# Performance work log

Hardware: AMD Instinct MI355X
Metric: run time of the kernel (lower is better)

Reference implementation:

```python
import jax, jax.numpy as jnp
import numpy as np

H, W, D = 56, 56, 28            # input_resolution
WS = (7, 7, 7)                  # window size (Wh, Ww, Wd)
SS = (3, 3, 3)                  # shift size
DIM = 96
NH = 3
HD = DIM // NH
N = WS[0] * WS[1] * WS[2]       # 343 tokens per window
NW = (H // WS[0]) * (W // WS[1]) * (D // WS[2])  # 256 windows


def _rel_pos_index():
    Wd, Wh, Ww = WS
    coords = np.stack(np.meshgrid(np.arange(Wd), np.arange(Wh), np.arange(Ww), indexing='ij'))
    cf = coords.reshape(3, -1)
    rel = (cf[:, :, None] - cf[:, None, :]).transpose(1, 2, 0)
    rel[:, :, 0] += Wd - 1
    rel[:, :, 1] += Wh - 1
    rel[:, :, 2] += Ww - 1
    rel[:, :, 0] *= (2 * Wh - 1) * (2 * Ww - 1)
    rel[:, :, 1] *= (2 * Ww - 1)
    return rel.sum(-1)  # (N, N)


def _attn_mask():
    img = np.zeros((H, W, D), np.float32)
    def slices(w, s):
        return (slice(0, -w), slice(-w, -s), slice(-s, None))
    cnt = 0
    for hs in slices(WS[0], SS[0]):
        for ws in slices(WS[1], SS[1]):
            for ds in slices(WS[2], SS[2]):
                img[hs, ws, ds] = cnt
                cnt += 1
    mw = img.reshape(H // WS[0], WS[0], W // WS[1], WS[1], D // WS[2], WS[2])
    mw = mw.transpose(0, 2, 4, 1, 3, 5).reshape(-1, N)  # (NW, N)
    am = mw[:, None, :] - mw[:, :, None]
    return np.where(am != 0, np.float32(-100.0), np.float32(0.0))


REL_IDX = jnp.asarray(_rel_pos_index())
ATTN_MASK = jnp.asarray(_attn_mask())  # (NW, N, N)


def _ln(x, g, b, eps=1e-5):
    m = x.mean(-1, keepdims=True)
    v = jnp.mean((x - m) ** 2, -1, keepdims=True)
    return (x - m) * jax.lax.rsqrt(v + eps) * g + b


def _forward(x, n1g, n1b, qkv_w, qkv_b, rpb, proj_w, proj_b,
             n2g, n2b, fc1_w, fc1_b, fc2_w, fc2_b):
    B, L, C = x.shape
    shortcut = x
    h = _ln(x, n1g, n1b).reshape(B, H, W, D, C)
    # cyclic shift
    h = jnp.roll(h, (-SS[0], -SS[1], -SS[2]), axis=(1, 2, 3))
    # window partition -> (B*NW, N, C)
    h = h.reshape(B, H // WS[0], WS[0], W // WS[1], WS[1], D // WS[2], WS[2], C)
    h = h.transpose(0, 1, 3, 5, 2, 4, 6, 7).reshape(-1, N, C)
    # qkv
    qkv = (h @ qkv_w + qkv_b).reshape(-1, N, 3, NH, HD).transpose(2, 0, 3, 1, 4)
    q, k, v = qkv[0] * (HD ** -0.5), qkv[1], qkv[2]  # (B*NW, NH, N, HD)
    attn = jnp.einsum('bhnd,bhmd->bhnm', q, k)
    bias = rpb[REL_IDX.reshape(-1)].reshape(N, N, NH).transpose(2, 0, 1)
    attn = attn + bias[None]
    # shifted-window mask
    attn = attn.reshape(B, NW, NH, N, N) + ATTN_MASK[None, :, None]
    attn = jax.nn.softmax(attn.reshape(-1, NH, N, N), axis=-1)
    o = jnp.einsum('bhnm,bhmd->bhnd', attn, v).transpose(0, 2, 1, 3).reshape(-1, N, C)
    o = o @ proj_w + proj_b
    # window reverse
    o = o.reshape(B, H // WS[0], W // WS[1], D // WS[2], WS[0], WS[1], WS[2], C)
    o = o.transpose(0, 1, 4, 2, 5, 3, 6, 7).reshape(B, H, W, D, C)
    o = jnp.roll(o, SS, axis=(1, 2, 3)).reshape(B, L, C)
    x = shortcut + o
    h2 = _ln(x, n2g, n2b)
    h2 = jax.nn.gelu(h2 @ fc1_w + fc1_b, approximate=False) @ fc2_w + fc2_b
    return x + h2


def setup_inputs() -> dict:
    key = jax.random.key(0)
    ks = jax.random.split(key, 6)
    C, FF = DIM, 4 * DIM
    f32 = jnp.float32
    return {
        'x': jax.random.normal(ks[0], (1, H * W * D, C), f32),
        'n1g': jnp.ones((C,), f32), 'n1b': jnp.zeros((C,), f32),
        'qkv_w': jax.random.normal(ks[1], (C, 3 * C), f32) * 0.02,
        'qkv_b': jnp.zeros((3 * C,), f32),
        'rpb': jax.random.normal(ks[2], ((2 * WS[0] - 1) * (2 * WS[1] - 1) * (2 * WS[2] - 1), NH), f32) * 0.02,
        'proj_w': jax.random.normal(ks[3], (C, C), f32) * 0.02,
        'proj_b': jnp.zeros((C,), f32),
        'n2g': jnp.ones((C,), f32), 'n2b': jnp.zeros((C,), f32),
        'fc1_w': jax.random.normal(ks[4], (C, FF), f32) * 0.02,
        'fc1_b': jnp.zeros((FF,), f32),
        'fc2_w': jax.random.normal(ks[5], (FF, C), f32) * 0.02,
        'fc2_b': jnp.zeros((C,), f32),
    }


def reference(x, n1g, n1b, qkv_w, qkv_b, rpb, proj_w, proj_b,
              n2g, n2b, fc1_w, fc1_b, fc2_w, fc2_b):
    return _forward(x, n1g, n1b, qkv_w, qkv_b, rpb, proj_w, proj_b,
                    n2g, n2b, fc1_w, fc1_b, fc2_w, fc2_b)
```

## Files before the change

kernel.cpp:

```cpp
#include <hip/hip_runtime.h>
#include <hip/hip_bf16.h>


#define L_TOK 87808

typedef unsigned int uint;
typedef __attribute__((ext_vector_type(8))) short short8;
typedef __attribute__((ext_vector_type(4))) float f32x4;

__device__ __forceinline__ float bflo(uint u){ union{uint x; float f;} a; a.x = u << 16; return a.f; }
__device__ __forceinline__ float bfhi(uint u){ union{uint x; float f;} a; a.x = u & 0xffff0000u; return a.f; }
__device__ __forceinline__ float bfval(unsigned short w){ union{uint x; float f;} a; a.x = (uint)w << 16; return a.f; }
__device__ __forceinline__ unsigned short f2bfbits(float f){
  union{float f; uint u;} a; a.f = f;
  uint u = a.u;
  u += 0x7fffu + ((u >> 16) & 1u);
  return (unsigned short)(u >> 16);
}
__device__ __forceinline__ unsigned short bfb(float f){
  __hip_bfloat16 h = __float2bfloat16(f);
  return *reinterpret_cast<unsigned short*>(&h);
}
__device__ __forceinline__ uint pkbf(float a, float b){
  return ((uint)bfb(b) << 16) | (uint)bfb(a);
}
__device__ __forceinline__ uint pack2(float a, float b){
  return ((uint)f2bfbits(b) << 16) | (uint)f2bfbits(a);
}
__device__ __forceinline__ uint4 pack8(const float* p){
  uint4 u;
  u.x = pack2(p[0], p[1]); u.y = pack2(p[2], p[3]);
  u.z = pack2(p[4], p[5]); u.w = pack2(p[6], p[7]);
  return u;
}
__device__ __forceinline__ uint4 pack8g(const float* gp){
  float t[8];
  *(float4*)&t[0] = *(const float4*)gp;
  *(float4*)&t[4] = *(const float4*)(gp + 4);
  return pack8(t);
}
__device__ __forceinline__ float gelu_f(float v){
  const float ax = fabsf(v) * 0.70710678118654752f;
  const float t  = 1.0f / (1.0f + 0.3275911f * ax);
  const float poly = t*(0.254829592f + t*(-0.284496736f + t*(1.421413741f +
                     t*(-1.453152027f + t*1.061405429f))));
  float erfv = 1.0f - poly * __expf(-ax*ax);
  erfv = copysignf(erfv, v);
  return 0.5f * v * (1.0f + erfv);
}
__device__ __forceinline__ uint gt_of_row(uint row){
  const uint win = row / 343u, n = row % 343u;
  const uint wh = win >> 5, ww = (win >> 2) & 7u, wd = win & 3u;
  const uint ih = n / 49u, rr = n % 49u, iw = rr / 7u, id = rr % 7u;
  uint gh = wh*7u + ih + 3u; if (gh >= 56u) gh -= 56u;
  uint gw = ww*7u + iw + 3u; if (gw >= 56u) gw -= 56u;
  uint gd = wd*7u + id + 3u; if (gd >= 28u) gd -= 28u;
  return ((gh*56u + gw)*28u + gd) * 96u;
}

__global__ __launch_bounds__(256)
void k_tr(const float* __restrict__ src, unsigned short* __restrict__ dst,
          int K, int N)
{
  const int idx = blockIdx.x * 256 + threadIdx.x;
  if (idx < K * N) {
    const int n = idx / K, k = idx % K;
    dst[idx] = f2bfbits(src[(size_t)k * N + n]);
  }
}

__global__ __launch_bounds__(256)
void k_mb(const float* __restrict__ rpbg, unsigned short* __restrict__ MB)
{
  const int idx = blockIdx.x * 256 + threadIdx.x;
  const int cls = idx / (3*352*352);
  const int rem = idx - cls * (3*352*352);
  const int h = rem / (352*352);
  const int rem2 = rem - h * (352*352);
  const int q = rem2 / 352;
  const int k = rem2 - q * 352;
  unsigned short v = 0xFF80;
  if (q < 343 && k < 343) {
    const int q0 = q/49, q1 = (q%49)/7, q2 = q%7;
    const int k0 = k/49, k1 = (k%49)/7, k2 = k%7;
    const int bq = q0*169 + q1*13 + q2;
    const int bk = k0*169 + k1*13 + k2;
    float bias = rpbg[(size_t)(bq - bk + 1098)*3 + h];
    int cq = 0, ck = 0;
    if (cls & 4) { cq += ((q0 < 4) ? 1 : 2)*9; ck += ((k0 < 4) ? 1 : 2)*9; }
    if (cls & 2) { cq += ((q1 < 4) ? 1 : 2)*3; ck += ((k1 < 4) ? 1 : 2)*3; }
    if (cls & 1) { cq += (q2 < 4) ? 1 : 2;     ck += (k2 < 4) ? 1 : 2; }
    if (cq != ck) bias -= 100.0f;
    v = f2bfbits(bias);
  }
  MB[idx] = v;
}

__global__ __launch_bounds__(256)
void k_qkv_ln(const float* __restrict__ x,
              const float* __restrict__ n1g,
              const float* __restrict__ n1b,
              const unsigned short* __restrict__ qkvwt,
              const float* __restrict__ bias, size_t headStride,
              __hip_bfloat16* __restrict__ qb,
              __hip_bfloat16* __restrict__ kb,
              __hip_bfloat16* __restrict__ vb)
{
  __shared__ __align__(16) unsigned short As[64][104];
  __shared__ uint srcOff[64];
  __shared__ float gLds[96], bLds[96];
  __shared__ float pSum[256], pSq[256];
  __shared__ float mLds[64], sLds[64];

  const int tid = threadIdx.x;
  const int wave = tid >> 6, lane = tid & 63;
  const int row0 = blockIdx.x * 64;

  if (tid < 64) srcOff[tid] = gt_of_row((uint)(row0 + tid));
  if (tid < 96) { gLds[tid] = n1g[tid]; bLds[tid] = n1b[tid]; }
  __syncthreads();

  for (int i = tid; i < 768; i += 256) {
    const int r = i / 12, kk = (i % 12) * 8;
    *(uint4*)&As[r][kk] = pack8g(x + srcOff[r] + kk);
  }
  __syncthreads();

  {
    const int r = tid & 63, seg = tid >> 6;
    float s = 0.0f, sq = 0.0f;
    #pragma unroll
    for (int j3 = 0; j3 < 3; ++j3) {
      const uint4 u = *(const uint4*)&As[r][seg*24 + j3*8];
      float v[8];
      v[0]=bflo(u.x); v[1]=bfhi(u.x); v[2]=bflo(u.y); v[3]=bfhi(u.y);
      v[4]=bflo(u.z); v[5]=bfhi(u.z); v[6]=bflo(u.w); v[7]=bfhi(u.w);
      #pragma unroll
      for (int j = 0; j < 8; ++j) { s += v[j]; sq += v[j]*v[j]; }
    }
    pSum[tid] = s; pSq[tid] = sq;
  }
  __syncthreads();
  if (tid < 64) {
    const float s  = pSum[tid] + pSum[tid+64] + pSum[tid+128] + pSum[tid+192];
    const float sq = pSq[tid] + pSq[tid+64] + pSq[tid+128] + pSq[tid+192];
    const float mean = s * (1.0f/96.0f);
    mLds[tid] = mean;
    sLds[tid] = rsqrtf(sq*(1.0f/96.0f) - mean*mean + 1e-5f);
  }
  __syncthreads();
  for (int i = tid; i < 768; i += 256) {
    const int r = i / 12, kk = (i % 12) * 8;
    uint4 u = *(uint4*)&As[r][kk];
    const float m = mLds[r], sc = sLds[r];
    float v[8];
    v[0]=bflo(u.x); v[1]=bfhi(u.x); v[2]=bflo(u.y); v[3]=bfhi(u.y);
    v[4]=bflo(u.z); v[5]=bfhi(u.z); v[6]=bflo(u.w); v[7]=bfhi(u.w);
    #pragma unroll
    for (int j = 0; j < 8; ++j) v[j] = (v[j] - m)*sc*gLds[kk+j] + bLds[kk+j];
    *(uint4*)&As[r][kk] = pack8(v);
  }
  __syncthreads();

  f32x4 acc[18];
  #pragma unroll
  for (int i = 0; i < 18; ++i) acc[i] = (f32x4){0.f, 0.f, 0.f, 0.f};
  const int ml = lane & 15, q8 = (lane >> 4) * 8;
  #pragma unroll
  for (int kc = 0; kc < 3; ++kc) {
    const short8 a = *(const short8*)&As[wave*16 + ml][kc*32 + q8];
    #pragma unroll
    for (int nt = 0; nt < 18; ++nt) {
      const short8 b = *(const short8*)(qkvwt + (size_t)(nt*16 + ml)*96 + kc*32 + q8);
      acc[nt] = __builtin_amdgcn_mfma_f32_16x16x32_bf16(a, b, acc[nt], 0, 0, 0);
    }
  }

  const float qscale = 0.17677669529663687f;
  #pragma unroll
  for (int nt = 0; nt < 18; ++nt) {
    const int nbase = nt * 16;
    const int part = nbase / 96;
    const int rem  = nbase - part * 96;
    const int h    = rem >> 5;
    const int dbase= rem & 31;
    __hip_bfloat16* base = (part == 0) ? qb : ((part == 1) ? kb : vb);
    __hip_bfloat16* dst = base + (size_t)h * headStride;
    const float bv = bias[nbase + ml];
    #pragma unroll
    for (int r = 0; r < 4; ++r) {
      const size_t row = (size_t)(row0 + wave*16 + (lane >> 4)*4 + r);
      float v = acc[nt][r] + bv;
      if (part == 0) v *= qscale;
      dst[row*32 + dbase + ml] = __float2bfloat16(v);
    }
  }
}

template<bool BF16OUT>
__global__ __launch_bounds__(256, 4)
void k_attn_v10(const __hip_bfloat16* __restrict__ qg,
                const __hip_bfloat16* __restrict__ kg,
                const __hip_bfloat16* __restrict__ vg,
                size_t headStride,
                const unsigned short* __restrict__ MB,
                void* __restrict__ obp)
{
  __shared__ __align__(16) unsigned short vt[32*344 + 16];
  __shared__ __align__(16) unsigned short Pc[4][16*56];
  __shared__ float lred[4][16];

  const int tid = threadIdx.x;
  const int wave = tid >> 6, lane = tid & 63;
  const uint win = blockIdx.x;
  const int hh = (int)blockIdx.y;
  const int mtBase = (int)blockIdx.z * 11;
  const size_t wbase = (size_t)hh * headStride + (size_t)win * (343*32);
  const unsigned short* qw = (const unsigned short*)qg + wbase;
  const unsigned short* kw = (const unsigned short*)kg + wbase;
  const unsigned short* vw = (const unsigned short*)vg + wbase;

  const uint wh = win >> 5, ww = (win >> 2) & 7u, wd = win & 3u;
  const int cls = ((wh == 7u) ? 4 : 0) | ((ww == 7u) ? 2 : 0) | ((wd == 3u) ? 1 : 0);
  const unsigned short* MBh = MB + ((size_t)cls*3 + hh) * (352*352);

  for (int t = tid; t < 343; t += 256) {
    const uint4* src = (const uint4*)(vw + (size_t)t*32);
    #pragma unroll
    for (int c4 = 0; c4 < 4; ++c4) {
      const uint4 u = src[c4];
      const int d = c4*8;
      vt[(d+0)*344 + t] = (unsigned short)(u.x & 0xffffu);
      vt[(d+1)*344 + t] = (unsigned short)(u.x >> 16);
      vt[(d+2)*344 + t] = (unsigned short)(u.y & 0xffffu);
      vt[(d+3)*344 + t] = (unsigned short)(u.y >> 16);
      vt[(d+4)*344 + t] = (unsigned short)(u.z & 0xffffu);
      vt[(d+5)*344 + t] = (unsigned short)(u.z >> 16);
      vt[(d+6)*344 + t] = (unsigned short)(u.w & 0xffffu);
      vt[(d+7)*344 + t] = (unsigned short)(u.w >> 16);
    }
  }
  if (tid < 32) vt[tid*344 + 343] = 0;
  if (tid < 16) vt[32*344 + tid] = 0;
  __syncthreads();

  const int ml = lane & 15, g = lane >> 4, g8 = g*8;
  unsigned short* Pw = &Pc[wave][0];

  for (int mt = mtBase + wave; mt < mtBase + 11; mt += 4) {
    const int q = mt*16 + ml;
    const short8 qf = *(const short8*)(qw + (size_t)q*32 + g8);
    const unsigned short* MBq = MBh + (size_t)q * 352;
    float l = 0.0f;
    f32x4 o0 = {0.f,0.f,0.f,0.f}, o1 = {0.f,0.f,0.f,0.f};

    for (int kc = 0; kc < 11; ++kc) {
      const short8 kf0 = *(const short8*)(kw + (size_t)(kc*32 + ml)*32 + g8);
      const short8 kf1 = *(const short8*)(kw + (size_t)(kc*32 + 16 + ml)*32 + g8);
      f32x4 s0 = __builtin_amdgcn_mfma_f32_16x16x32_bf16(kf0, qf, (f32x4){0.f,0.f,0.f,0.f}, 0, 0, 0);
      f32x4 s1 = __builtin_amdgcn_mfma_f32_16x16x32_bf16(kf1, qf, (f32x4){0.f,0.f,0.f,0.f}, 0, 0, 0);

      const ushort4 u0 = *(const ushort4*)(MBq + kc*32 + 4*g);
      const ushort4 u1 = *(const ushort4*)(MBq + kc*32 + 16 + 4*g);

      float p0 = __expf(s0[0] + bfval(u0.x));
      float p1 = __expf(s0[1] + bfval(u0.y));
      float p2 = __expf(s0[2] + bfval(u0.z));
      float p3 = __expf(s0[3] + bfval(u0.w));
      float p4 = __expf(s1[0] + bfval(u1.x));
      float p5 = __expf(s1[1] + bfval(u1.y));
      float p6 = __expf(s1[2] + bfval(u1.z));
      float p7 = __expf(s1[3] + bfval(u1.w));
      l += ((p0 + p1) + (p2 + p3)) + ((p4 + p5) + (p6 + p7));

      uint2 wlo, whi;
      wlo.x = pkbf(p0, p1); wlo.y = pkbf(p2, p3);
      whi.x = pkbf(p4, p5); whi.y = pkbf(p6, p7);
      *(uint2*)&Pw[ml*56 + 4*g]      = wlo;
      *(uint2*)&Pw[ml*56 + 16 + 4*g] = whi;

      const short8 pf  = *(const short8*)&Pw[ml*56 + g8];
      const short8 vf0 = *(const short8*)&vt[(size_t)ml*344 + kc*32 + g8];
      const short8 vf1 = *(const short8*)&vt[(size_t)(16 + ml)*344 + kc*32 + g8];
      o0 = __builtin_amdgcn_mfma_f32_16x16x32_bf16(pf, vf0, o0, 0, 0, 0);
      o1 = __builtin_amdgcn_mfma_f32_16x16x32_bf16(pf, vf1, o1, 0, 0, 0);
    }

    l += __shfl_xor(l, 16);
    l += __shfl_xor(l, 32);
    if (g == 0) lred[wave][ml] = 1.0f / l;
    const float4 li = *(const float4*)&lred[wave][4*g];
    #pragma unroll
    for (int r = 0; r < 4; ++r) {
      const int row = mt*16 + 4*g + r;
      if (row < 343) {
        const size_t base = ((size_t)win*343 + (uint)row)*96 + hh*32;
        if (BF16OUT) {
          __hip_bfloat16* op = (__hip_bfloat16*)obp + base;
          op[ml]      = __float2bfloat16(o0[r] * li[r]);
          op[16 + ml] = __float2bfloat16(o1[r] * li[r]);
        } else {
          float* op = (float*)obp + base;
          op[ml]      = o0[r] * li[r];
          op[16 + ml] = o1[r] * li[r];
        }
      }
    }
  }
}

__global__ __launch_bounds__(256, 2)
void k_pm(const __hip_bfloat16* __restrict__ obb,
          const unsigned short* __restrict__ pwt,
          const float* __restrict__ pb,
          const float* __restrict__ xin,
          const float* __restrict__ n2g,
          const float* __restrict__ n2b,
          const unsigned short* __restrict__ w1t,
          const float* __restrict__ b1,
          const unsigned short* __restrict__ w2t,
          const float* __restrict__ b2,
          float* __restrict__ out)
{
  __shared__ __align__(16) unsigned short As[64][104];
  __shared__ __align__(16) unsigned short Rs[64][104];
  __shared__ __align__(16) unsigned short inter[64][200];
  __shared__ uint gtO[64];
  float* scr  = (float*)&inter[0][0];
  float* pSum = scr;
  float* pSq  = scr + 256;
  float* gL   = scr + 512;
  float* bL   = scr + 608;
  float* mL   = scr + 704;
  float* sL   = scr + 768;

  const int tid = threadIdx.x;
  const int wave = tid >> 6, lane = tid & 63;
  const int row0 = blockIdx.x * 64;
  const int ml = lane & 15, g = lane >> 4, g8 = g*8;

  if (tid < 64) gtO[tid] = gt_of_row((uint)(row0 + tid));
  if (tid < 96) { gL[tid] = n2g[tid]; bL[tid] = n2b[tid]; }
  for (int i = tid; i < 768; i += 256) {
    const int r = i / 12, kk = (i % 12) * 8;
    *(uint4*)&As[r][kk] = *(const uint4*)(obb + (size_t)(row0 + r)*96 + kk);
  }
  __syncthreads();

  {
    short8 paf[3];
    #pragma unroll
    for (int kc = 0; kc < 3; ++kc)
      paf[kc] = *(const short8*)&As[wave*16 + ml][kc*32 + g8];
    f32x4 acc[6];
    #pragma unroll
    for (int i = 0; i < 6; ++i) acc[i] = (f32x4){0.f, 0.f, 0.f, 0.f};
    #pragma unroll
    for (int kc = 0; kc < 3; ++kc)
      #pragma unroll
      for (int nt = 0; nt < 6; ++nt) {
        const short8 b = *(const short8*)(pwt + (size_t)(nt*16 + ml)*96 + kc*32 + g8);
        acc[nt] = __builtin_amdgcn_mfma_f32_16x16x32_bf16(paf[kc], b, acc[nt], 0, 0, 0);
      }
    #pragma unroll
    for (int nt = 0; nt < 6; ++nt) {
      const int col = nt*16 + ml;
      const float pbv = pb[col];
      #pragma unroll
      for (int r = 0; r < 4; ++r) {
        const int rl = wave*16 + 4*g + r;
        const float v = acc[nt][r] + pbv + xin[(size_t)gtO[rl] + col];
        Rs[rl][col] = f2bfbits(v);
      }
    }
  }
  __syncthreads();

  {
    const int r = tid & 63, seg = tid >> 6;
    float s = 0.0f, sq = 0.0f;
    #pragma unroll
    for (int j3 = 0; j3 < 3; ++j3) {
      const uint4 u = *(const uint4*)&Rs[r][seg*24 + j3*8];
      float v[8];
      v[0]=bflo(u.x); v[1]=bfhi(u.x); v[2]=bflo(u.y); v[3]=bfhi(u.y);
      v[4]=bflo(u.z); v[5]=bfhi(u.z); v[6]=bflo(u.w); v[7]=bfhi(u.w);
      #pragma unroll
      for (int j = 0; j < 8; ++j) { s += v[j]; sq += v[j]*v[j]; }
    }
    pSum[tid] = s; pSq[tid] = sq;
  }
  __syncthreads();
  if (tid < 64) {
    const float s  = pSum[tid] + pSum[tid+64] + pSum[tid+128] + pSum[tid+192];
    const float sq = pSq[tid] + pSq[tid+64] + pSq[tid+128] + pSq[tid+192];
    const float mean = s * (1.0f/96.0f);
    mL[tid] = mean;
    sL[tid] = rsqrtf(sq*(1.0f/96.0f) - mean*mean + 1e-5f);
  }
  __syncthreads();
  for (int i = tid; i < 768; i += 256) {
    const int r = i / 12, kk = (i % 12) * 8;
    uint4 u = *(uint4*)&Rs[r][kk];
    const float m = mL[r], sc = sL[r];
    float v[8];
    v[0]=bflo(u.x); v[1]=bfhi(u.x); v[2]=bflo(u.y); v[3]=bfhi(u.y);
    v[4]=bflo(u.z); v[5]=bfhi(u.z); v[6]=bflo(u.w); v[7]=bfhi(u.w);
    #pragma unroll
    for (int j = 0; j < 8; ++j) v[j] = (v[j] - m)*sc*gL[kk+j] + bL[kk+j];
    *(uint4*)&As[r][kk] = pack8(v);
  }
  __syncthreads();

  short8 af[4][3];
  #pragma unroll
  for (int mt = 0; mt < 4; ++mt)
    #pragma unroll
    for (int kc = 0; kc < 3; ++kc)
      af[mt][kc] = *(const short8*)&As[mt*16 + ml][kc*32 + g8];

  const int rb = 32 * (wave >> 1);
  const int cb = 48 * (wave & 1);
  f32x4 acc2[2][3];
  #pragma unroll
  for (int i = 0; i < 2; ++i)
    #pragma unroll
    for (int nt = 0; nt < 3; ++nt)
      acc2[i][nt] = (f32x4){0.f, 0.f, 0.f, 0.f};

  #pragma unroll
  for (int H = 0; H < 2; ++H) {
    if (H) __syncthreads();

    const int nbg = H*192 + 48*wave;
    const int cl0 = 48*wave;
    short8 bf[3][3];
    #pragma unroll
    for (int nt = 0; nt < 3; ++nt)
      #pragma unroll
      for (int kc = 0; kc < 3; ++kc)
        bf[nt][kc] = *(const short8*)(w1t + (size_t)(nbg + 16*nt + ml)*96 + kc*32 + g8);

    f32x4 acc[4][3];
    #pragma unroll
    for (int mt = 0; mt < 4; ++mt)
      #pragma unroll
      for (int nt = 0; nt < 3; ++nt)
        acc[mt][nt] = (f32x4){0.f, 0.f, 0.f, 0.f};

    #pragma unroll
    for (int kc = 0; kc < 3; ++kc)
      #pragma unroll
      for (int nt = 0; nt < 3; ++nt)
        #pragma unroll
        for (int mt = 0; mt < 4; ++mt)
          acc[mt][nt] = __builtin_amdgcn_mfma_f32_16x16x32_bf16(af[mt][kc], bf[nt][kc], acc[mt][nt], 0, 0, 0);

    #pragma unroll
    for (int nt = 0; nt < 3; ++nt) {
      const float b1v = b1[nbg + 16*nt + ml];
      const int c = cl0 + 16*nt + ml;
      #pragma unroll
      for (int mt = 0; mt < 4; ++mt) {
        #pragma unroll
        for (int r = 0; r < 4; ++r) {
          inter[mt*16 + 4*g + r][c] = f2bfbits(gelu_f(acc[mt][nt][r] + b1v));
        }
      }
    }
    __syncthreads();

    #pragma unroll
    for (int kcl = 0; kcl < 6; ++kcl) {
      const short8 a0 = *(const short8*)&inter[rb + ml][kcl*32 + g8];
      const short8 a1 = *(const short8*)&inter[rb + 16 + ml][kcl*32 + g8];
      #pragma unroll
      for (int nt = 0; nt < 3; ++nt) {
        const short8 b = *(const short8*)(w2t + (size_t)(cb + 16*nt + ml)*384 + H*192 + kcl*32 + g8);
        acc2[0][nt] = __builtin_amdgcn_mfma_f32_16x16x32_bf16(a0, b, acc2[0][nt], 0, 0, 0);
        acc2[1][nt] = __builtin_amdgcn_mfma_f32_16x16x32_bf16(a1, b, acc2[1][nt], 0, 0, 0);
      }
    }
  }

  #pragma unroll
  for (int i = 0; i < 2; ++i) {
    #pragma unroll
    for (int nt = 0; nt < 3; ++nt) {
      const int col = cb + 16*nt + ml;
      const float b2v = b2[col];
      #pragma unroll
      for (int r = 0; r < 4; ++r) {
        const int rl = rb + 16*i + 4*g + r;
        out[(size_t)gtO[rl] + col] = acc2[i][nt][r] + b2v + bfval(Rs[rl][col]);
      }
    }
  }
}

__global__ __launch_bounds__(256)
void k_proj(const float* __restrict__ A,
            const unsigned short* __restrict__ pwt,
            const float* __restrict__ bias,
            const float* __restrict__ xin,
            __hip_bfloat16* __restrict__ xres)
{
  __shared__ __align__(16) unsigned short As[128][104];
  const int tid = threadIdx.x;
  const int wave = tid >> 6, lane = tid & 63;
  const int row0 = blockIdx.x * 128;

  for (int i = tid; i < 1536; i += 256) {
    const int r = i / 12, kk = (i % 12) * 8;
    *(uint4*)&As[r][kk] = pack8g(A + (size_t)(row0 + r)*96 + kk);
  }
  __syncthreads();

  f32x4 acc[2][6];
  #pragma unroll
  for (int mt = 0; mt < 2; ++mt)
    #pragma unroll
    for (int i = 0; i < 6; ++i) acc[mt][i] = (f32x4){0.f, 0.f, 0.f, 0.f};
  const int ml = lane & 15, q8 = (lane >> 4) * 8;
  #pragma unroll
  for (int kc = 0; kc < 3; ++kc) {
    const short8 a0 = *(const short8*)&As[wave*32 + ml][kc*32 + q8];
    const short8 a1 = *(const short8*)&As[wave*32 + 16 + ml][kc*32 + q8];
    #pragma unroll
    for (int nt = 0; nt < 6; ++nt) {
      const short8 b = *(const short8*)(pwt + (size_t)(nt*16 + ml)*96 + kc*32 + q8);
      acc[0][nt] = __builtin_amdgcn_mfma_f32_16x16x32_bf16(a0, b, acc[0][nt], 0, 0, 0);
      acc[1][nt] = __builtin_amdgcn_mfma_f32_16x16x32_bf16(a1, b, acc[1][nt], 0, 0, 0);
    }
  }

  #pragma unroll
  for (int mt = 0; mt < 2; ++mt) {
    #pragma unroll
    for (int r = 0; r < 4; ++r) {
      const uint row = (uint)(row0 + wave*32 + mt*16 + (lane >> 4)*4 + r);
      const size_t gt = (size_t)gt_of_row(row);
      #pragma unroll
      for (int nt = 0; nt < 6; ++nt) {
        const int col = nt*16 + ml;
        xres[gt + col] = __float2bfloat16(acc[mt][nt][r] + bias[col] + xin[gt + col]);
      }
    }
  }
}

__global__ __launch_bounds__(256, 4)
void k_mlp(const __hip_bfloat16* __restrict__ xresb,
           const float* __restrict__ n2g,
           const float* __restrict__ n2b,
           const unsigned short* __restrict__ w1t,
           const float* __restrict__ b1,
           const unsigned short* __restrict__ w2t,
           const float* __restrict__ b2,
           float* __restrict__ out)
{
  __shared__ __align__(16) unsigned short As[64][104];
  __shared__ __align__(16) unsigned short inter[64][200];
  float* scr  = (float*)&inter[0][0];
  float* pSum = scr;
  float* pSq  = scr + 256;
  float* gL   = scr + 512;
  float* bL   = scr + 608;
  float* mL   = scr + 704;
  float* sL   = scr + 768;

  const int tid = threadIdx.x;
  const int wave = tid >> 6, lane = tid & 63;
  const int row0 = blockIdx.x * 64;
  const int ml = lane & 15, g = lane >> 4, g8 = g*8;

  if (tid < 96) { gL[tid] = n2g[tid]; bL[tid] = n2b[tid]; }
  for (int i = tid; i < 768; i += 256) {
    const int r = i / 12, kk = (i % 12) * 8;
    *(uint4*)&As[r][kk] = *(const uint4*)(xresb + (size_t)(row0 + r)*96 + kk);
  }
  __syncthreads();

  {
    const int r = tid & 63, seg = tid >> 6;
    float s = 0.0f, sq = 0.0f;
    #pragma unroll
    for (int j3 = 0; j3 < 3; ++j3) {
      const uint4 u = *(const uint4*)&As[r][seg*24 + j3*8];
      float v[8];
      v[0]=bflo(u.x); v[1]=bfhi(u.x); v[2]=bflo(u.y); v[3]=bfhi(u.y);
      v[4]=bflo(u.z); v[5]=bfhi(u.z); v[6]=bflo(u.w); v[7]=bfhi(u.w);
      #pragma unroll
      for (int j = 0; j < 8; ++j) { s += v[j]; sq += v[j]*v[j]; }
    }
    pSum[tid] = s; pSq[tid] = sq;
  }
  __syncthreads();
  if (tid < 64) {
    const float s  = pSum[tid] + pSum[tid+64] + pSum[tid+128] + pSum[tid+192];
    const float sq = pSq[tid] + pSq[tid+64] + pSq[tid+128] + pSq[tid+192];
    const float mean = s * (1.0f/96.0f);
    mL[tid] = mean;
    sL[tid] = rsqrtf(sq*(1.0f/96.0f) - mean*mean + 1e-5f);
  }
  __syncthreads();
  for (int i = tid; i < 768; i += 256) {
    const int r = i / 12, kk = (i % 12) * 8;
    uint4 u = *(uint4*)&As[r][kk];
    const float m = mL[r], sc = sL[r];
    float v[8];
    v[0]=bflo(u.x); v[1]=bfhi(u.x); v[2]=bflo(u.y); v[3]=bfhi(u.y);
    v[4]=bflo(u.z); v[5]=bfhi(u.z); v[6]=bflo(u.w); v[7]=bfhi(u.w);
    #pragma unroll
    for (int j = 0; j < 8; ++j) v[j] = (v[j] - m)*sc*gL[kk+j] + bL[kk+j];
    *(uint4*)&As[r][kk] = pack8(v);
  }
  __syncthreads();

  short8 af[4][3];
  #pragma unroll
  for (int mt = 0; mt < 4; ++mt)
    #pragma unroll
    for (int kc = 0; kc < 3; ++kc)
      af[mt][kc] = *(const short8*)&As[mt*16 + ml][kc*32 + g8];

  const int rb = 32 * (wave >> 1);
  const int cb = 48 * (wave & 1);
  f32x4 acc2[2][3];
  #pragma unroll
  for (int i = 0; i < 2; ++i)
    #pragma unroll
    for (int nt = 0; nt < 3; ++nt)
      acc2[i][nt] = (f32x4){0.f, 0.f, 0.f, 0.f};

  #pragma unroll
  for (int H = 0; H < 2; ++H) {
    if (H) __syncthreads();

    const int nbg = H*192 + 48*wave;
    const int cl0 = 48*wave;
    short8 bf[3][3];
    #pragma unroll
    for (int nt = 0; nt < 3; ++nt)
      #pragma unroll
      for (int kc = 0; kc < 3; ++kc)
        bf[nt][kc] = *(const short8*)(w1t + (size_t)(nbg + 16*nt + ml)*96 + kc*32 + g8);

    f32x4 acc[4][3];
    #pragma unroll
    for (int mt = 0; mt < 4; ++mt)
      #pragma unroll
      for (int nt = 0; nt < 3; ++nt)
        acc[mt][nt] = (f32x4){0.f, 0.f, 0.f, 0.f};

    #pragma unroll
    for (int kc = 0; kc < 3; ++kc)
      #pragma unroll
      for (int nt = 0; nt < 3; ++nt)
        #pragma unroll
        for (int mt = 0; mt < 4; ++mt)
          acc[mt][nt] = __builtin_amdgcn_mfma_f32_16x16x32_bf16(af[mt][kc], bf[nt][kc], acc[mt][nt], 0, 0, 0);

    #pragma unroll
    for (int nt = 0; nt < 3; ++nt) {
      const float b1v = b1[nbg + 16*nt + ml];
      const int c = cl0 + 16*nt + ml;
      #pragma unroll
      for (int mt = 0; mt < 4; ++mt) {
        #pragma unroll
        for (int r = 0; r < 4; ++r) {
          inter[mt*16 + 4*g + r][c] = f2bfbits(gelu_f(acc[mt][nt][r] + b1v));
        }
      }
    }
    __syncthreads();

    #pragma unroll
    for (int kcl = 0; kcl < 6; ++kcl) {
      const short8 a0 = *(const short8*)&inter[rb + ml][kcl*32 + g8];
      const short8 a1 = *(const short8*)&inter[rb + 16 + ml][kcl*32 + g8];
      #pragma unroll
      for (int nt = 0; nt < 3; ++nt) {
        const short8 b = *(const short8*)(w2t + (size_t)(cb + 16*nt + ml)*384 + H*192 + kcl*32 + g8);
        acc2[0][nt] = __builtin_amdgcn_mfma_f32_16x16x32_bf16(a0, b, acc2[0][nt], 0, 0, 0);
        acc2[1][nt] = __builtin_amdgcn_mfma_f32_16x16x32_bf16(a1, b, acc2[1][nt], 0, 0, 0);
      }
    }
  }

  const unsigned short* xu = (const unsigned short*)xresb;
  #pragma unroll
  for (int i = 0; i < 2; ++i) {
    #pragma unroll
    for (int nt = 0; nt < 3; ++nt) {
      const int col = cb + 16*nt + ml;
      const float b2v = b2[col];
      #pragma unroll
      for (int r = 0; r < 4; ++r) {
        const size_t row = (size_t)(row0 + rb + 16*i + 4*g + r);
        out[row*96 + col] = acc2[i][nt][r] + b2v + bfval(xu[row*96 + col]);
      }
    }
  }
}

extern "C" void kernel_launch(void* const* d_in, const int* in_sizes, int n_in,
                              void* d_out, int out_size, void* d_ws, size_t ws_size,
                              hipStream_t stream)
{
  (void)in_sizes; (void)n_in; (void)out_size;
  const float* x    = (const float*)d_in[0];
  const float* n1g  = (const float*)d_in[1];
  const float* n1b  = (const float*)d_in[2];
  const float* qkvw = (const float*)d_in[3];
  const float* qkvb = (const float*)d_in[4];
  const float* rpb  = (const float*)d_in[5];
  const float* pw   = (const float*)d_in[6];
  const float* pb   = (const float*)d_in[7];
  const float* n2g  = (const float*)d_in[8];
  const float* n2b  = (const float*)d_in[9];
  const float* f1w  = (const float*)d_in[10];
  const float* f1b  = (const float*)d_in[11];
  const float* f2w  = (const float*)d_in[12];
  const float* f2b  = (const float*)d_in[13];
  float* out = (float*)d_out;

  const size_t E = (size_t)L_TOK * 96;
  __hip_bfloat16* qb = (__hip_bfloat16*)d_ws;
  __hip_bfloat16* kb = qb + E;
  __hip_bfloat16* vb = kb + E;
  __hip_bfloat16* xres = (__hip_bfloat16*)d_ws;
  const size_t hs = (size_t)L_TOK * 32;

  unsigned short* qkvwt = (unsigned short*)d_out;
  unsigned short* pwt   = (unsigned short*)kb;
  unsigned short* w1t   = pwt + 9216;
  unsigned short* w2t   = w1t + 36864;

  const size_t MB_BYTES = (size_t)8 * 3 * 352 * 352 * 2;
  const bool mbok  = ws_size >= (size_t)6 * E + MB_BYTES;
  const bool fused = ws_size >= (size_t)8 * E + MB_BYTES;
  unsigned short* MBp = mbok ? (unsigned short*)((char*)d_ws + (size_t)6 * E) : nullptr;
  __hip_bfloat16* obb = fused ? (__hip_bfloat16*)((char*)d_ws + (size_t)6 * E + MB_BYTES) : nullptr;

  if (MBp) k_mb<<<11616, 256, 0, stream>>>(rpb, MBp);

  k_tr<<<108, 256, 0, stream>>>(qkvw, qkvwt, 96, 288);
  k_qkv_ln<<<L_TOK/64, 256, 0, stream>>>(
      x, n1g, n1b, qkvwt, qkvb, hs, qb, kb, vb);

  if (fused && MBp) {
    k_attn_v10<true><<<dim3(256, 3, 2), 256, 0, stream>>>(qb, kb, vb, hs, MBp, (void*)obb);
    k_tr<<<36, 256, 0, stream>>>(pw, pwt, 96, 96);
    k_tr<<<144, 256, 0, stream>>>(f1w, w1t, 96, 384);
    k_tr<<<144, 256, 0, stream>>>(f2w, w2t, 384, 96);
    k_pm<<<L_TOK/64, 256, 0, stream>>>(obb, pwt, pb, x, n2g, n2b,
                                       w1t, f1b, w2t, f2b, out);
  } else {
    float* ob = out;
    k_attn_v10<false><<<dim3(256, 3, 2), 256, 0, stream>>>(qb, kb, vb, hs, MBp, (void*)ob);
    k_tr<<<36, 256, 0, stream>>>(pw, pwt, 96, 96);
    k_tr<<<144, 256, 0, stream>>>(f1w, w1t, 96, 384);
    k_tr<<<144, 256, 0, stream>>>(f2w, w2t, 384, 96);
    k_proj<<<L_TOK/128, 256, 0, stream>>>(ob, pwt, pb, x, xres);
    k_mlp<<<L_TOK/64, 256, 0, stream>>>(xres, n2g, n2b, w1t, f1b, w2t, f2b, out);
  }
}
```

Baseline: 276.8 us.

## Merge weight transposes into one launch and restructure proj+MLP kernel

```diff
diff --git a/kernel.cpp b/kernel.cpp
--- a/kernel.cpp
+++ b/kernel.cpp
@@ -63,6 +63,24 @@
           int K, int N)
 {
   const int idx = blockIdx.x * 256 + threadIdx.x;
+  if (idx < K * N) {
+    const int n = idx / K, k = idx % K;
+    dst[idx] = f2bfbits(src[(size_t)k * N + n]);
+  }
+}
+
+__global__ __launch_bounds__(256)
+void k_tr4(const float* __restrict__ qkvw, unsigned short* __restrict__ qkvwt,
+           const float* __restrict__ pw,   unsigned short* __restrict__ pwt,
+           const float* __restrict__ f1w,  unsigned short* __restrict__ w1t,
+           const float* __restrict__ f2w,  unsigned short* __restrict__ w2t)
+{
+  const int b = blockIdx.x, tid = threadIdx.x;
+  const float* src; unsigned short* dst; int K, N, idx;
+  if (b < 108)      { src = qkvw; dst = qkvwt; K = 96;  N = 288; idx = b*256 + tid; }
+  else if (b < 144) { src = pw;   dst = pwt;   K = 96;  N = 96;  idx = (b-108)*256 + tid; }
+  else if (b < 288) { src = f1w;  dst = w1t;   K = 96;  N = 384; idx = (b-144)*256 + tid; }
+  else              { src = f2w;  dst = w2t;   K = 384; N = 96;  idx = (b-288)*256 + tid; }
   if (idx < K * N) {
     const int n = idx / K, k = idx % K;
     dst[idx] = f2bfbits(src[(size_t)k * N + n]);
@@ -309,7 +327,7 @@
   }
 }
 
-__global__ __launch_bounds__(256, 2)
+__global__ __launch_bounds__(256, 3)
 void k_pm(const __hip_bfloat16* __restrict__ obb,
           const unsigned short* __restrict__ pwt,
           const float* __restrict__ pb,
@@ -326,89 +344,91 @@
   __shared__ __align__(16) unsigned short Rs[64][104];
   __shared__ __align__(16) unsigned short inter[64][200];
   __shared__ uint gtO[64];
-  float* scr  = (float*)&inter[0][0];
-  float* pSum = scr;
-  float* pSq  = scr + 256;
-  float* gL   = scr + 512;
-  float* bL   = scr + 608;
-  float* mL   = scr + 704;
-  float* sL   = scr + 768;
 
   const int tid = threadIdx.x;
   const int wave = tid >> 6, lane = tid & 63;
   const int row0 = blockIdx.x * 64;
   const int ml = lane & 15, g = lane >> 4, g8 = g*8;
 
+  uint gtr[4];
+  #pragma unroll
+  for (int r = 0; r < 4; ++r) gtr[r] = gt_of_row((uint)(row0 + wave*16 + 4*g + r));
+  float xv[4][6];
+  #pragma unroll
+  for (int r = 0; r < 4; ++r)
+    #pragma unroll
+    for (int nt = 0; nt < 6; ++nt)
+      xv[r][nt] = xin[(size_t)gtr[r] + nt*16 + ml];
+  float pbv[6], gv[6], bvv[6];
+  #pragma unroll
+  for (int nt = 0; nt < 6; ++nt) {
+    pbv[nt] = pb[nt*16 + ml];
+    gv[nt]  = n2g[nt*16 + ml];
+    bvv[nt] = n2b[nt*16 + ml];
+  }
+  float b1a[3], b1b[3], b2v[3];
+  const int cbp = 48 * (wave & 1);
+  #pragma unroll
+  for (int nt = 0; nt < 3; ++nt) {
+    b1a[nt] = b1[48*wave + 16*nt + ml];
+    b1b[nt] = b1[192 + 48*wave + 16*nt + ml];
+    b2v[nt] = b2[cbp + 16*nt + ml];
+  }
   if (tid < 64) gtO[tid] = gt_of_row((uint)(row0 + tid));
-  if (tid < 96) { gL[tid] = n2g[tid]; bL[tid] = n2b[tid]; }
   for (int i = tid; i < 768; i += 256) {
     const int r = i / 12, kk = (i % 12) * 8;
     *(uint4*)&As[r][kk] = *(const uint4*)(obb + (size_t)(row0 + r)*96 + kk);
   }
   __syncthreads();
 
-  {
-    short8 paf[3];
+  f32x4 acc[6];
+  #pragma unroll
+  for (int i = 0; i < 6; ++i) acc[i] = (f32x4){0.f, 0.f, 0.f, 0.f};
+  #pragma unroll
+  for (int kc = 0; kc < 3; ++kc) {
+    const short8 a = *(const short8*)&As[wave*16 + ml][kc*32 + g8];
+    #pragma unroll
+    for (int nt = 0; nt < 6; ++nt) {
+      const short8 b = *(const short8*)(pwt + (size_t)(nt*16 + ml)*96 + kc*32 + g8);
+      acc[nt] = __builtin_amdgcn_mfma_f32_16x16x32_bf16(a, b, acc[nt], 0, 0, 0);
+    }
+  }
+
+  short8 bf[3][3];
+  #pragma unroll
+  for (int nt = 0; nt < 3; ++nt)
     #pragma unroll
     for (int kc = 0; kc < 3; ++kc)
-      paf[kc] = *(const short8*)&As[wave*16 + ml][kc*32 + g8];
-    f32x4 acc[6];
-    #pragma unroll
-    for (int i = 0; i < 6; ++i) acc[i] = (f32x4){0.f, 0.f, 0.f, 0.f};
-    #pragma unroll
-    for (int kc = 0; kc < 3; ++kc)
-      #pragma unroll
-      for (int nt = 0; nt < 6; ++nt) {
-        const short8 b = *(const short8*)(pwt + (size_t)(nt*16 + ml)*96 + kc*32 + g8);
-        acc[nt] = __builtin_amdgcn_mfma_f32_16x16x32_bf16(paf[kc], b, acc[nt], 0, 0, 0);
-      }
+      bf[nt][kc] = *(const short8*)(w1t + (size_t)(48*wave + 16*nt + ml)*96 + kc*32 + g8);
+
+  float vr[4][6];
+  float s[4] = {0.f,0.f,0.f,0.f}, sq[4] = {0.f,0.f,0.f,0.f};
+  #pragma unroll
+  for (int r = 0; r < 4; ++r) {
+    const int row = wave*16 + 4*g + r;
     #pragma unroll
     for (int nt = 0; nt < 6; ++nt) {
-      const int col = nt*16 + ml;
-      const float pbv = pb[col];
-      #pragma unroll
-      for (int r = 0; r < 4; ++r) {
-        const int rl = wave*16 + 4*g + r;
-        const float v = acc[nt][r] + pbv + xin[(size_t)gtO[rl] + col];
-        Rs[rl][col] = f2bfbits(v);
-      }
-    }
-  }
-  __syncthreads();
-
-  {
-    const int r = tid & 63, seg = tid >> 6;
-    float s = 0.0f, sq = 0.0f;
-    #pragma unroll
-    for (int j3 = 0; j3 < 3; ++j3) {
-      const uint4 u = *(const uint4*)&Rs[r][seg*24 + j3*8];
-      float v[8];
-      v[0]=bflo(u.x); v[1]=bfhi(u.x); v[2]=bflo(u.y); v[3]=bfhi(u.y);
-      v[4]=bflo(u.z); v[5]=bfhi(u.z); v[6]=bflo(u.w); v[7]=bfhi(u.w);
-      #pragma unroll
-      for (int j = 0; j < 8; ++j) { s += v[j]; sq += v[j]*v[j]; }
-    }
-    pSum[tid] = s; pSq[tid] = sq;
-  }
-  __syncthreads();
-  if (tid < 64) {
-    const float s  = pSum[tid] + pSum[tid+64] + pSum[tid+128] + pSum[tid+192];
-    const float sq = pSq[tid] + pSq[tid+64] + pSq[tid+128] + pSq[tid+192];
-    const float mean = s * (1.0f/96.0f);
-    mL[tid] = mean;
-    sL[tid] = rsqrtf(sq*(1.0f/96.0f) - mean*mean + 1e-5f);
-  }
-  __syncthreads();
-  for (int i = tid; i < 768; i += 256) {
-    const int r = i / 12, kk = (i % 12) * 8;
-    uint4 u = *(uint4*)&Rs[r][kk];
-    const float m = mL[r], sc = sL[r];
-    float v[8];
-    v[0]=bflo(u.x); v[1]=bfhi(u.x); v[2]=bflo(u.y); v[3]=bfhi(u.y);
-    v[4]=bflo(u.z); v[5]=bfhi(u.z); v[6]=bflo(u.w); v[7]=bfhi(u.w);
-    #pragma unroll
-    for (int j = 0; j < 8; ++j) v[j] = (v[j] - m)*sc*gL[kk+j] + bL[kk+j];
-    *(uint4*)&As[r][kk] = pack8(v);
+      const float v = acc[nt][r] + pbv[nt] + xv[r][nt];
+      const unsigned short ub = f2bfbits(v);
+      Rs[row][nt*16 + ml] = ub;
+      const float vv = bfval(ub);
+      vr[r][nt] = vv;
+      s[r] += vv; sq[r] += vv*vv;
+    }
+  }
+  #pragma unroll
+  for (int r = 0; r < 4; ++r) {
+    #pragma unroll
+    for (int m = 1; m <= 8; m <<= 1) {
+      s[r]  += __shfl_xor(s[r],  m);
+      sq[r] += __shfl_xor(sq[r], m);
+    }
+    const float mean = s[r] * (1.0f/96.0f);
+    const float rstd = rsqrtf(sq[r]*(1.0f/96.0f) - mean*mean + 1e-5f);
+    const int row = wave*16 + 4*g + r;
+    #pragma unroll
+    for (int nt = 0; nt < 6; ++nt)
+      As[row][nt*16 + ml] = f2bfbits((vr[r][nt] - mean)*rstd*gv[nt] + bvv[nt]);
   }
   __syncthreads();
 
@@ -420,7 +440,7 @@
       af[mt][kc] = *(const short8*)&As[mt*16 + ml][kc*32 + g8];
 
   const int rb = 32 * (wave >> 1);
-  const int cb = 48 * (wave & 1);
+  const int cb = cbp;
   f32x4 acc2[2][3];
   #pragma unroll
   for (int i = 0; i < 2; ++i)
@@ -428,58 +448,90 @@
     for (int nt = 0; nt < 3; ++nt)
       acc2[i][nt] = (f32x4){0.f, 0.f, 0.f, 0.f};
 
-  #pragma unroll
-  for (int H = 0; H < 2; ++H) {
-    if (H) __syncthreads();
-
-    const int nbg = H*192 + 48*wave;
-    const int cl0 = 48*wave;
-    short8 bf[3][3];
-    #pragma unroll
-    for (int nt = 0; nt < 3; ++nt)
-      #pragma unroll
-      for (int kc = 0; kc < 3; ++kc)
-        bf[nt][kc] = *(const short8*)(w1t + (size_t)(nbg + 16*nt + ml)*96 + kc*32 + g8);
-
-    f32x4 acc[4][3];
+  short8 bf1[3][3];
+
+  {
+    f32x4 a1[4][3];
     #pragma unroll
     for (int mt = 0; mt < 4; ++mt)
       #pragma unroll
       for (int nt = 0; nt < 3; ++nt)
-        acc[mt][nt] = (f32x4){0.f, 0.f, 0.f, 0.f};
-
+        a1[mt][nt] = (f32x4){0.f, 0.f, 0.f, 0.f};
     #pragma unroll
     for (int kc = 0; kc < 3; ++kc)
       #pragma unroll
       for (int nt = 0; nt < 3; ++nt)
         #pragma unroll
         for (int mt = 0; mt < 4; ++mt)
-          acc[mt][nt] = __builtin_amdgcn_mfma_f32_16x16x32_bf16(af[mt][kc], bf[nt][kc], acc[mt][nt], 0, 0, 0);
+          a1[mt][nt] = __builtin_amdgcn_mfma_f32_16x16x32_bf16(af[mt][kc], bf[nt][kc], a1[mt][nt], 0, 0, 0);
+
+    #pragma unroll
+    for (int nt = 0; nt < 3; ++nt)
+      #pragma unroll
+      for (int kc = 0; kc < 3; ++kc)
+        bf1[nt][kc] = *(const short8*)(w1t + (size_t)(192 + 48*wave + 16*nt + ml)*96 + kc*32 + g8);
 
     #pragma unroll
     for (int nt = 0; nt < 3; ++nt) {
-      const float b1v = b1[nbg + 16*nt + ml];
-      const int c = cl0 + 16*nt + ml;
-      #pragma unroll
-      for (int mt = 0; mt < 4; ++mt) {
+      const int c = 48*wave + 16*nt + ml;
+      #pragma unroll
+      for (int mt = 0; mt < 4; ++mt)
         #pragma unroll
-        for (int r = 0; r < 4; ++r) {
-          inter[mt*16 + 4*g + r][c] = f2bfbits(gelu_f(acc[mt][nt][r] + b1v));
-        }
-      }
-    }
-    __syncthreads();
-
-    #pragma unroll
-    for (int kcl = 0; kcl < 6; ++kcl) {
-      const short8 a0 = *(const short8*)&inter[rb + ml][kcl*32 + g8];
-      const short8 a1 = *(const short8*)&inter[rb + 16 + ml][kcl*32 + g8];
-      #pragma unroll
-      for (int nt = 0; nt < 3; ++nt) {
-        const short8 b = *(const short8*)(w2t + (size_t)(cb + 16*nt + ml)*384 + H*192 + kcl*32 + g8);
-        acc2[0][nt] = __builtin_amdgcn_mfma_f32_16x16x32_bf16(a0, b, acc2[0][nt], 0, 0, 0);
-        acc2[1][nt] = __builtin_amdgcn_mfma_f32_16x16x32_bf16(a1, b, acc2[1][nt], 0, 0, 0);
-      }
+        for (int r = 0; r < 4; ++r)
+          inter[mt*16 + 4*g + r][c] = f2bfbits(gelu_f(a1[mt][nt][r] + b1a[nt]));
+    }
+  }
+  __syncthreads();
+
+  #pragma unroll
+  for (int kcl = 0; kcl < 6; ++kcl) {
+    const short8 a0 = *(const short8*)&inter[rb + ml][kcl*32 + g8];
+    const short8 a1 = *(const short8*)&inter[rb + 16 + ml][kcl*32 + g8];
+    #pragma unroll
+    for (int nt = 0; nt < 3; ++nt) {
+      const short8 b = *(const short8*)(w2t + (size_t)(cb + 16*nt + ml)*384 + kcl*32 + g8);
+      acc2[0][nt] = __builtin_amdgcn_mfma_f32_16x16x32_bf16(a0, b, acc2[0][nt], 0, 0, 0);
+      acc2[1][nt] = __builtin_amdgcn_mfma_f32_16x16x32_bf16(a1, b, acc2[1][nt], 0, 0, 0);
+    }
+  }
+  __syncthreads();
+
+  {
+    f32x4 a1[4][3];
+    #pragma unroll
+    for (int mt = 0; mt < 4; ++mt)
+      #pragma unroll
+      for (int nt = 0; nt < 3; ++nt)
+        a1[mt][nt] = (f32x4){0.f, 0.f, 0.f, 0.f};
+    #pragma unroll
+    for (int kc = 0; kc < 3; ++kc)
+      #pragma unroll
+      for (int nt = 0; nt < 3; ++nt)
+        #pragma unroll
+        for (int mt = 0; mt < 4; ++mt)
+          a1[mt][nt] = __builtin_amdgcn_mfma_f32_16x16x32_bf16(af[mt][kc], bf1[nt][kc], a1[mt][nt], 0, 0, 0);
+
+    #pragma unroll
+    for (int nt = 0; nt < 3; ++nt) {
+      const int c = 48*wave + 16*nt + ml;
+      #pragma unroll
+      for (int mt = 0; mt < 4; ++mt)
+        #pragma unroll
+        for (int r = 0; r < 4; ++r)
+          inter[mt*16 + 4*g + r][c] = f2bfbits(gelu_f(a1[mt][nt][r] + b1b[nt]));
+    }
+  }
+  __syncthreads();
+
+  #pragma unroll
+  for (int kcl = 0; kcl < 6; ++kcl) {
+    const short8 a0 = *(const short8*)&inter[rb + ml][kcl*32 + g8];
+    const short8 a1 = *(const short8*)&inter[rb + 16 + ml][kcl*32 + g8];
+    #pragma unroll
+    for (int nt = 0; nt < 3; ++nt) {
+      const short8 b = *(const short8*)(w2t + (size_t)(cb + 16*nt + ml)*384 + 192 + kcl*32 + g8);
+      acc2[0][nt] = __builtin_amdgcn_mfma_f32_16x16x32_bf16(a0, b, acc2[0][nt], 0, 0, 0);
+      acc2[1][nt] = __builtin_amdgcn_mfma_f32_16x16x32_bf16(a1, b, acc2[1][nt], 0, 0, 0);
     }
   }
 
@@ -488,11 +540,10 @@
     #pragma unroll
     for (int nt = 0; nt < 3; ++nt) {
       const int col = cb + 16*nt + ml;
-      const float b2v = b2[col];
       #pragma unroll
       for (int r = 0; r < 4; ++r) {
         const int rl = rb + 16*i + 4*g + r;
-        out[(size_t)gtO[rl] + col] = acc2[i][nt][r] + b2v + bfval(Rs[rl][col]);
+        out[(size_t)gtO[rl] + col] = acc2[i][nt][r] + b2v[nt] + bfval(Rs[rl][col]);
       }
     }
   }
@@ -733,36 +784,51 @@
   const size_t hs = (size_t)L_TOK * 32;
 
   unsigned short* qkvwt = (unsigned short*)d_out;
-  unsigned short* pwt   = (unsigned short*)kb;
-  unsigned short* w1t   = pwt + 9216;
-  unsigned short* w2t   = w1t + 36864;
 
   const size_t MB_BYTES = (size_t)8 * 3 * 352 * 352 * 2;
-  const bool mbok  = ws_size >= (size_t)6 * E + MB_BYTES;
-  const bool fused = ws_size >= (size_t)8 * E + MB_BYTES;
-  unsigned short* MBp = mbok ? (unsigned short*)((char*)d_ws + (size_t)6 * E) : nullptr;
-  __hip_bfloat16* obb = fused ? (__hip_bfloat16*)((char*)d_ws + (size_t)6 * E + MB_BYTES) : nullptr;
+  const size_t WT_BYTES = (size_t)(9216 + 36864 + 36864) * 2;
+  const size_t off_mb  = (size_t)6 * E;
+  const size_t off_obb = off_mb + MB_BYTES;
+  const size_t off_wt  = off_obb + (size_t)2 * E;
+  const bool mbok  = ws_size >= off_obb;
+  const bool fused = ws_size >= off_wt;
+  const bool tier1 = ws_size >= off_wt + WT_BYTES;
+
+  unsigned short* MBp = mbok ? (unsigned short*)((char*)d_ws + off_mb) : nullptr;
+  __hip_bfloat16* obb = fused ? (__hip_bfloat16*)((char*)d_ws + off_obb) : nullptr;
 
   if (MBp) k_mb<<<11616, 256, 0, stream>>>(rpb, MBp);
 
-  k_tr<<<108, 256, 0, stream>>>(qkvw, qkvwt, 96, 288);
-  k_qkv_ln<<<L_TOK/64, 256, 0, stream>>>(
-      x, n1g, n1b, qkvwt, qkvb, hs, qb, kb, vb);
-
-  if (fused && MBp) {
+  if (tier1) {
+    unsigned short* pwt = (unsigned short*)((char*)d_ws + off_wt);
+    unsigned short* w1t = pwt + 9216;
+    unsigned short* w2t = w1t + 36864;
+    k_tr4<<<432, 256, 0, stream>>>(qkvw, qkvwt, pw, pwt, f1w, w1t, f2w, w2t);
+    k_qkv_ln<<<L_TOK/64, 256, 0, stream>>>(x, n1g, n1b, qkvwt, qkvb, hs, qb, kb, vb);
     k_attn_v10<true><<<dim3(256, 3, 2), 256, 0, stream>>>(qb, kb, vb, hs, MBp, (void*)obb);
-    k_tr<<<36, 256, 0, stream>>>(pw, pwt, 96, 96);
-    k_tr<<<144, 256, 0, stream>>>(f1w, w1t, 96, 384);
-    k_tr<<<144, 256, 0, stream>>>(f2w, w2t, 384, 96);
     k_pm<<<L_TOK/64, 256, 0, stream>>>(obb, pwt, pb, x, n2g, n2b,
                                        w1t, f1b, w2t, f2b, out);
   } else {
-    float* ob = out;
-    k_attn_v10<false><<<dim3(256, 3, 2), 256, 0, stream>>>(qb, kb, vb, hs, MBp, (void*)ob);
-    k_tr<<<36, 256, 0, stream>>>(pw, pwt, 96, 96);
-    k_tr<<<144, 256, 0, stream>>>(f1w, w1t, 96, 384);
-    k_tr<<<144, 256, 0, stream>>>(f2w, w2t, 384, 96);
-    k_proj<<<L_TOK/128, 256, 0, stream>>>(ob, pwt, pb, x, xres);
-    k_mlp<<<L_TOK/64, 256, 0, stream>>>(xres, n2g, n2b, w1t, f1b, w2t, f2b, out);
-  }
-}
+    unsigned short* pwt = (unsigned short*)kb;
+    unsigned short* w1t = pwt + 9216;
+    unsigned short* w2t = w1t + 36864;
+    k_tr<<<108, 256, 0, stream>>>(qkvw, qkvwt, 96, 288);
+    k_qkv_ln<<<L_TOK/64, 256, 0, stream>>>(x, n1g, n1b, qkvwt, qkvb, hs, qb, kb, vb);
+    if (fused) {
+      k_attn_v10<true><<<dim3(256, 3, 2), 256, 0, stream>>>(qb, kb, vb, hs, MBp, (void*)obb);
+      k_tr<<<36, 256, 0, stream>>>(pw, pwt, 96, 96);
+      k_tr<<<144, 256, 0, stream>>>(f1w, w1t, 96, 384);
+      k_tr<<<144, 256, 0, stream>>>(f2w, w2t, 384, 96);
+      k_pm<<<L_TOK/64, 256, 0, stream>>>(obb, pwt, pb, x, n2g, n2b,
+                                         w1t, f1b, w2t, f2b, out);
+    } else {
+      float* ob = out;
+      k_attn_v10<false><<<dim3(256, 3, 2), 256, 0, stream>>>(qb, kb, vb, hs, MBp, (void*)ob);
+      k_tr<<<36, 256, 0, stream>>>(pw, pwt, 96, 96);
+      k_tr<<<144, 256, 0, stream>>>(f1w, w1t, 96, 384);
+      k_tr<<<144, 256, 0, stream>>>(f2w, w2t, 384, 96);
+      k_proj<<<L_TOK/128, 256, 0, stream>>>(ob, pwt, pb, x, xres);
+      k_mlp<<<L_TOK/64, 256, 0, stream>>>(xres, n2g, n2b, w1t, f1b, w2t, f2b, out);
+    }
+  }
+}
```

Result: no change. 272.3 us (-1.6%).
